# Kernel optimization log

Measured on AMD Instinct MI355X. Metric: run time of the kernel, lower is better.

## Reference

```python
import jax, jax.numpy as jnp
import numpy as np

EMBED_DIM = 768
HEAD_DIM = 64
BATCH = 8
SEQ = 4096


def setup_inputs() -> dict:
    key = jax.random.key(0)
    k_x, k_q, k_k, k_v = jax.random.split(key, 4)
    input_ids = jax.random.normal(k_x, (BATCH, SEQ, EMBED_DIM), dtype=jnp.float32)
    # nn.Linear(embed, head, bias=False): weight shape [head, embed]; y = x @ W.T
    scale = 1.0 / np.sqrt(EMBED_DIM)
    Wq = jax.random.normal(k_q, (HEAD_DIM, EMBED_DIM), dtype=jnp.float32) * scale
    Wk = jax.random.normal(k_k, (HEAD_DIM, EMBED_DIM), dtype=jnp.float32) * scale
    Wv = jax.random.normal(k_v, (HEAD_DIM, EMBED_DIM), dtype=jnp.float32) * scale
    return {"input_ids": input_ids, "Wq": Wq, "Wk": Wk, "Wv": Wv}


def reference(input_ids, Wq, Wk, Wv):
    # Projections. NOTE: the original module (faithfully reproduced) computes
    # v with q_net, so Wv is unused in the forward math.
    q = jnp.einsum('bse,he->bsh', input_ids, Wq)  # [B,S,H]
    k = jnp.einsum('bse,he->bsh', input_ids, Wk)  # [B,S,H]
    v = jnp.einsum('bse,he->bsh', input_ids, Wq)  # bug in source: uses q_net
    seq_len = q.shape[1]
    # Non-standard scaling: divide by sqrt(seq_len), not sqrt(head_dim)
    scores = jnp.einsum('bqh,bkh->bqk', q, k) / jnp.sqrt(jnp.float32(seq_len))
    # Non-standard softmax axis: over the query axis (dim=1)
    attn_weights = jax.nn.softmax(scores, axis=1)  # [B,Sq,Sk]
    return jnp.einsum('bqk,bkh->bqh', attn_weights, v)
```

## Files before the change

kernel.cpp:

```cpp
#include <hip/hip_runtime.h>
#include <hip/hip_bf16.h>
#include <cstdint>


#define BATCH 8
#define SEQ   4096
#define EMB   768
#define HD    64
#define NROW  (BATCH*SEQ)

#define QSCALE 0.1803368801111201f
#define KSCALE 0.125f
#define CSCALE 5.545177444479562f

typedef float  f32x4  __attribute__((ext_vector_type(4)));
typedef float  f32x16 __attribute__((ext_vector_type(16)));
typedef __bf16 bf16x8 __attribute__((ext_vector_type(8)));
typedef unsigned short u16x8_t __attribute__((ext_vector_type(8)));
typedef unsigned int   u32x4_t __attribute__((ext_vector_type(4)));

__device__ __forceinline__ f32x4 mfma16(bf16x8 a, bf16x8 b, f32x4 c) {
  return __builtin_amdgcn_mfma_f32_16x16x32_bf16(a, b, c, 0, 0, 0);
}
__device__ __forceinline__ f32x16 mfma32(bf16x8 a, bf16x8 b, f32x16 c) {
  return __builtin_amdgcn_mfma_f32_32x32x16_bf16(a, b, c, 0, 0, 0);
}
__device__ __forceinline__ unsigned short f2b(float f) {
  __bf16 h = (__bf16)f;
  return __builtin_bit_cast(unsigned short, h);
}
__device__ __forceinline__ float b2f(unsigned short u) {
  unsigned int x = ((unsigned int)u) << 16;
  return __builtin_bit_cast(float, x);
}
__device__ __forceinline__ bf16x8 ldsA(const unsigned short* p) {
  return __builtin_bit_cast(bf16x8, *(const u16x8_t*)p);
}
__device__ __forceinline__ float expf2(float x) {
  float r; asm("v_exp_f32 %0, %1" : "=v"(r) : "v"(x)); return r;
}
__device__ __forceinline__ unsigned cvtpk(float lo, float hi) {
  unsigned r; asm("v_cvt_pk_bf16_f32 %0, %1, %2" : "=v"(r) : "v"(lo), "v"(hi)); return r;
}
__device__ __forceinline__ void plane32swap(unsigned &a, unsigned &b) {
  asm volatile("v_permlane32_swap_b32 %0, %1" : "+v"(a), "+v"(b));
}
__device__ __forceinline__ void glld16(const void* g, void* l) {
  __builtin_amdgcn_global_load_lds(
      (const __attribute__((address_space(1))) void*)g,
      (__attribute__((address_space(3))) void*)l, 16, 0, 0);
}
__device__ __forceinline__ int sidx(int r, int h) {
  return r * 64 + (h ^ ((r & 7) << 3));
}

__global__ __launch_bounds__(256) void wcvt_kernel(
    const float* __restrict__ Wq, const float* __restrict__ Wk,
    unsigned short* __restrict__ Wb) {
  int ci = blockIdx.x * 256 + threadIdx.x;
  int r = ci / 96, c8 = ci % 96;
  const float* src = (r < 64 ? Wq + (size_t)r * EMB : Wk + (size_t)(r - 64) * EMB) + c8 * 8;
  float4 a = *(const float4*)src, d = *(const float4*)(src + 4);
  u16x8_t o;
  o[0]=f2b(a.x); o[1]=f2b(a.y); o[2]=f2b(a.z); o[3]=f2b(a.w);
  o[4]=f2b(d.x); o[5]=f2b(d.y); o[6]=f2b(d.z); o[7]=f2b(d.w);
  *(u16x8_t*)(Wb + (size_t)ci * 8) = o;
}

__global__ __launch_bounds__(256) void proj_kernel(
    const float* __restrict__ X, const unsigned short* __restrict__ Wb,
    unsigned short* __restrict__ Qb, unsigned short* __restrict__ Kb) {
  __shared__ unsigned short Ws[2][8192];
  const int t = threadIdx.x, lane = t & 63, w = t >> 6;
  const int c = lane & 15, g = lane >> 4;
  const int row0 = blockIdx.x * 64;
  f32x4 acc[8];
#pragma unroll
  for (int f = 0; f < 8; ++f) { acc[f][0]=0.f; acc[f][1]=0.f; acc[f][2]=0.f; acc[f][3]=0.f; }

  auto STAGE = [&](int ec, int bb) {
#pragma unroll
    for (int i = 0; i < 4; ++i) {
      int rr = w + 4 * i;
      int ci = rr * 64 + lane;
      int r = ci >> 3, cL = ci & 7;
      glld16(Wb + (size_t)r * EMB + ec * 64 + (cL ^ (r & 7)) * 8, (void*)&Ws[bb][rr * 512]);
    }
  };
  STAGE(0, 0);
  __syncthreads();
  for (int ec = 0; ec < 12; ++ec) {
    if (ec < 11) STAGE(ec + 1, (ec + 1) & 1);
    bf16x8 Af[2];
#pragma unroll
    for (int es = 0; es < 2; ++es) {
      const float* xp = X + (size_t)(row0 + 16 * w + c) * EMB + ec * 64 + es * 32 + 8 * g;
      float4 v0 = *(const float4*)xp, v1 = *(const float4*)(xp + 4);
      u16x8_t tmp;
      tmp[0]=f2b(v0.x); tmp[1]=f2b(v0.y); tmp[2]=f2b(v0.z); tmp[3]=f2b(v0.w);
      tmp[4]=f2b(v1.x); tmp[5]=f2b(v1.y); tmp[6]=f2b(v1.z); tmp[7]=f2b(v1.w);
      Af[es] = __builtin_bit_cast(bf16x8, tmp);
    }
    const unsigned short* Wt = Ws[ec & 1];
#pragma unroll
    for (int es = 0; es < 2; ++es)
#pragma unroll
      for (int f = 0; f < 8; ++f) {
        bf16x8 Bf = ldsA(&Wt[sidx(16 * f + c, es * 32 + 8 * g)]);
        acc[f] = mfma16(Af[es], Bf, acc[f]);
      }
    __syncthreads();
  }
#pragma unroll
  for (int f = 0; f < 8; ++f) {
    int n = 16 * f + c;
    float sc = (n < 64) ? QSCALE : KSCALE;
#pragma unroll
    for (int r = 0; r < 4; ++r) {
      int ROW = row0 + 16 * w + 4 * g + r;
      unsigned short bv = f2b(acc[f][r] * sc);
      if (n < 64) Qb[(size_t)ROW * 64 + n] = bv;
      else        Kb[(size_t)ROW * 64 + (n - 64)] = bv;
    }
  }
}

__global__ __launch_bounds__(256) void colsum_kernel(
    const unsigned short* __restrict__ Qb, const unsigned short* __restrict__ Kb,
    float* __restrict__ Zpart) {
  __shared__ unsigned short Qs[2][8192];
  const int t = threadIdx.x, lane = t & 63, w = t >> 6;
  const int c = lane & 31, hi = lane >> 5;
  const int fid = blockIdx.x;
  const int b = fid & 7, rem = fid >> 3;
  const int kt = rem & 15, qs = rem >> 4;
  const size_t kbase = (size_t)b * SEQ + kt * 256;
  const size_t qbase0 = (size_t)b * SEQ + qs * 1024;

  bf16x8 Kf[2][4];
#pragma unroll
  for (int j = 0; j < 2; ++j)
#pragma unroll
    for (int es = 0; es < 4; ++es)
      Kf[j][es] = __builtin_bit_cast(bf16x8,
          *(const u16x8_t*)(Kb + (kbase + 64 * w + 32 * j + c) * 64 + 16 * es + 8 * hi));

  auto STAGE = [&](int qi, int bb) {
#pragma unroll
    for (int i = 0; i < 4; ++i) {
      int rr = w + 4 * i;
      int ci = rr * 64 + lane;
      int r = ci >> 3, cL = ci & 7;
      glld16(Qb + (qbase0 + qi * 128 + r) * 64 + (cL ^ (r & 7)) * 8, (void*)&Qs[bb][rr * 512]);
    }
  };
  float csum[2] = {0.f, 0.f};
  STAGE(0, 0);
  __syncthreads();
  for (int qi = 0; qi < 8; ++qi) {
    if (qi < 7) STAGE(qi + 1, (qi + 1) & 1);
    const unsigned short* Qt = Qs[qi & 1];
#pragma unroll
    for (int sq = 0; sq < 4; ++sq) {
      bf16x8 A[4];
#pragma unroll
      for (int es = 0; es < 4; ++es)
        A[es] = ldsA(&Qt[sidx(32 * sq + c, 16 * es + 8 * hi)]);
#pragma unroll
      for (int j = 0; j < 2; ++j) {
        f32x16 sv;
#pragma unroll
        for (int i = 0; i < 16; ++i) sv[i] = 0.f;
#pragma unroll
        for (int es = 0; es < 4; ++es) sv = mfma32(A[es], Kf[j][es], sv);
#pragma unroll
        for (int i = 0; i < 16; ++i) csum[j] += expf2(sv[i]);
      }
    }
    __syncthreads();
  }
#pragma unroll
  for (int j = 0; j < 2; ++j) {
    float v = csum[j] + __shfl_xor(csum[j], 32);
    if (lane < 32)
      Zpart[(kbase + 64 * w + 32 * j + lane) * 4 + qs] = v;
  }
}

__global__ __launch_bounds__(256) void vtrans_kernel(
    const unsigned short* __restrict__ Qb, const float* __restrict__ Zpart,
    unsigned short* __restrict__ VT) {
  __shared__ unsigned short T[128 * 72];
  __shared__ float cvs[128];
  const int t = threadIdx.x;
  const int kt = blockIdx.x, b = blockIdx.y;
  const size_t kbase = (size_t)b * SEQ + kt * 128;
#pragma unroll
  for (int it = 0; it < 4; ++it) {
    int ci = t + 256 * it;
    int r = ci >> 3, ch = ci & 7;
    u16x8_t v = *(const u16x8_t*)(Qb + (kbase + r) * 64 + 8 * ch);
    *(u16x8_t*)(&T[r * 72 + 8 * (ch ^ ((r >> 3) & 7))]) = v;
  }
  if (t < 128) {
    const float* zp = Zpart + (kbase + t) * 4;
    cvs[t] = CSCALE / (zp[0] + zp[1] + zp[2] + zp[3]);
  }
  __syncthreads();
#pragma unroll
  for (int it = 0; it < 4; ++it) {
    int ci = t + 256 * it;
    int h = ci >> 4, c16 = ci & 15;
    u16x8_t o;
#pragma unroll
    for (int j = 0; j < 8; ++j) {
      int r = 8 * c16 + j;
      unsigned short raw = T[r * 72 + 8 * ((h >> 3) ^ (c16 & 7)) + (h & 7)];
      o[j] = f2b(cvs[r] * b2f(raw));
    }
    *(u16x8_t*)(VT + ((size_t)(b * 64 + h)) * SEQ + kt * 128 + 8 * c16) = o;
  }
}

__global__ __launch_bounds__(256) void attn_kernel(
    const unsigned short* __restrict__ Qb, const unsigned short* __restrict__ Kb,
    const unsigned short* __restrict__ VT, float* __restrict__ outp, int nkt) {
  __shared__ unsigned short KV[2][16384];
  const int t = threadIdx.x, lane = t & 63, w = t >> 6;
  const int c = lane & 31, hi = lane >> 5;
  const int fid = blockIdx.x;
  const int b = fid & 7, rem = fid >> 3;
  const int qt = rem & 15, ks = rem >> 4;
  const size_t brow = (size_t)b * SEQ;
  const int q0 = qt * 256;
  const int koff = ks * nkt;

  bf16x8 Qf[2][4];
#pragma unroll
  for (int j = 0; j < 2; ++j)
#pragma unroll
    for (int es = 0; es < 4; ++es)
      Qf[j][es] = __builtin_bit_cast(bf16x8,
          *(const u16x8_t*)(Qb + (brow + q0 + 64 * w + 32 * j + c) * 64 + 16 * es + 8 * hi));

  f32x16 acc[2][2];
#pragma unroll
  for (int j = 0; j < 2; ++j)
#pragma unroll
    for (int hb = 0; hb < 2; ++hb)
#pragma unroll
      for (int i = 0; i < 16; ++i) acc[j][hb][i] = 0.f;

  auto STAGE = [&](int tt, int bb) {
    const size_t kb0 = brow + (size_t)(koff + tt) * 128;
#pragma unroll
    for (int i = 0; i < 8; ++i) {
      int rr = w + 4 * i;
      int ci = rr * 64 + lane;
      if (rr < 16) {
        int r = ci >> 3, cL = ci & 7;
        glld16(Kb + (kb0 + r) * 64 + (cL ^ (r & 7)) * 8, (void*)&KV[bb][rr * 512]);
      } else {
        int jj = ci - 1024;
        int h = jj >> 4, cL = jj & 15;
        glld16(VT + ((size_t)(b * 64 + h)) * SEQ + (size_t)(koff + tt) * 128 +
                   (cL ^ (h & 7)) * 8,
               (void*)&KV[bb][rr * 512]);
      }
    }
  };

  auto COMPUTE = [&](int bb) {
    const unsigned short* Ks = &KV[bb][0];
    const unsigned short* Vs = &KV[bb][8192];
#pragma unroll
    for (int kb = 0; kb < 4; ++kb) {
      bf16x8 KA[4];
#pragma unroll
      for (int es = 0; es < 4; ++es)
        KA[es] = ldsA(&Ks[sidx(32 * kb + c, 16 * es + 8 * hi)]);
      bf16x8 fA[2][2];
#pragma unroll
      for (int j = 0; j < 2; ++j) {
        f32x16 sv;
#pragma unroll
        for (int i = 0; i < 16; ++i) sv[i] = 0.f;
#pragma unroll
        for (int es = 0; es < 4; ++es) sv = mfma32(KA[es], Qf[j][es], sv);
        float p[16];
#pragma unroll
        for (int i = 0; i < 16; ++i) p[i] = expf2(sv[i]);
        unsigned X0 = cvtpk(p[0], p[1]),  X1 = cvtpk(p[2], p[3]);
        unsigned Y0 = cvtpk(p[4], p[5]),  Y1 = cvtpk(p[6], p[7]);
        plane32swap(X0, Y0); plane32swap(X1, Y1);
        u32x4_t F0 = {X0, X1, Y0, Y1};
        unsigned Z0 = cvtpk(p[8], p[9]),   Z1 = cvtpk(p[10], p[11]);
        unsigned W0 = cvtpk(p[12], p[13]), W1 = cvtpk(p[14], p[15]);
        plane32swap(Z0, W0); plane32swap(Z1, W1);
        u32x4_t F1 = {Z0, Z1, W0, W1};
        fA[j][0] = __builtin_bit_cast(bf16x8, F0);
        fA[j][1] = __builtin_bit_cast(bf16x8, F1);
      }
#pragma unroll
      for (int hb = 0; hb < 2; ++hb) {
        int h = 32 * hb + c;
        int col0 = 32 * kb + 8 * hi;
        bf16x8 VB0 = ldsA(&Vs[h * 128 + (col0 ^ ((h & 7) << 3))]);
        bf16x8 VB1 = ldsA(&Vs[h * 128 + ((col0 + 16) ^ ((h & 7) << 3))]);
        acc[0][hb] = mfma32(fA[0][0], VB0, acc[0][hb]);
        acc[0][hb] = mfma32(fA[0][1], VB1, acc[0][hb]);
        acc[1][hb] = mfma32(fA[1][0], VB0, acc[1][hb]);
        acc[1][hb] = mfma32(fA[1][1], VB1, acc[1][hb]);
      }
    }
  };

  STAGE(0, 0);
  __syncthreads();
  for (int tt = 0; tt < nkt; ++tt) {
    if (tt + 1 < nkt) STAGE(tt + 1, (tt + 1) & 1);
    COMPUTE(tt & 1);
    __syncthreads();
  }
  float* op = outp + (size_t)ks * NROW * 64;
#pragma unroll
  for (int j = 0; j < 2; ++j)
#pragma unroll
    for (int hb = 0; hb < 2; ++hb)
#pragma unroll
      for (int r = 0; r < 16; ++r) {
        int qrow = (r & 3) + 8 * (r >> 2) + 4 * hi;
        op[(brow + q0 + 64 * w + 32 * j + qrow) * 64 + 32 * hb + c] = acc[j][hb][r];
      }
}

__global__ __launch_bounds__(256) void osum_kernel(
    const float4* __restrict__ A, const float4* __restrict__ B,
    const float4* __restrict__ C, const float4* __restrict__ D,
    float4* __restrict__ O) {
  int i = blockIdx.x * 256 + threadIdx.x;
  float4 x = A[i], y = B[i], z = C[i], u = D[i];
  float4 o;
  o.x = (x.x + y.x) + (z.x + u.x);
  o.y = (x.y + y.y) + (z.y + u.y);
  o.z = (x.z + y.z) + (z.z + u.z);
  o.w = (x.w + y.w) + (z.w + u.w);
  O[i] = o;
}

extern "C" void kernel_launch(void* const* d_in, const int* in_sizes, int n_in,
                              void* d_out, int out_size, void* d_ws, size_t ws_size,
                              hipStream_t stream) {
  const float* X  = (const float*)d_in[0];
  const float* Wq = (const float*)d_in[1];
  const float* Wk = (const float*)d_in[2];
  float* Out = (float*)d_out;

  unsigned char* wsb = (unsigned char*)d_ws;
  const size_t QB_OFF = 0;
  const size_t KB_OFF = 4194304;
  const size_t WB_OFF = 8388608;
  const size_t Z_OFF  = 8585216;
  const size_t VT_OFF = 9240576;
  const size_t OP_OFF = 13434880;
  const size_t TOTAL_SPLIT = OP_OFF + (size_t)4 * NROW * 64 * 4;

  unsigned short* Qb = (unsigned short*)(wsb + QB_OFF);
  unsigned short* Kb = (unsigned short*)(wsb + KB_OFF);
  unsigned short* Wb = (unsigned short*)(wsb + WB_OFF);
  float* Zpart       = (float*)(wsb + Z_OFF);
  unsigned short* VT = (unsigned short*)(wsb + VT_OFF);
  float* Opart       = (float*)(wsb + OP_OFF);

  const bool split = (ws_size >= TOTAL_SPLIT);

  hipLaunchKernelGGL(wcvt_kernel, dim3(48), dim3(256), 0, stream, Wq, Wk, Wb);
  hipLaunchKernelGGL(proj_kernel, dim3(NROW / 64), dim3(256), 0, stream, X, Wb, Qb, Kb);
  hipLaunchKernelGGL(colsum_kernel, dim3(512), dim3(256), 0, stream, Qb, Kb, Zpart);
  hipLaunchKernelGGL(vtrans_kernel, dim3(32, 8), dim3(256), 0, stream, Qb, Zpart, VT);
  if (split) {
    hipLaunchKernelGGL(attn_kernel, dim3(512), dim3(256), 0, stream,
                       Qb, Kb, VT, Opart, 8);
    const size_t PS = (size_t)NROW * 64;
    hipLaunchKernelGGL(osum_kernel, dim3(2048), dim3(256), 0, stream,
                       (const float4*)Opart, (const float4*)(Opart + PS),
                       (const float4*)(Opart + 2 * PS), (const float4*)(Opart + 3 * PS),
                       (float4*)Out);
  } else {
    hipLaunchKernelGGL(attn_kernel, dim3(128), dim3(256), 0, stream,
                       Qb, Kb, VT, Out, 32);
  }
}
```

Baseline: 105.5 us.

## Store split-K attention partials as fp16 and halve K/V tile size

The split-K attention kernel now writes its four partial outputs in fp16 instead of fp32, and the reduction kernel reads fp16 partials with 8-wide vector loads. This halves the partial-output traffic on both the write and the read side. The key/value LDS tile also shrinks from 128 to 64 keys per stage with twice as many iterations, which cuts shared memory per block and may allow more resident blocks, at the cost of more barriers. Rounding the partials to fp16 adds some precision loss.

```diff
diff --git a/kernel.cpp b/kernel.cpp
--- a/kernel.cpp
+++ b/kernel.cpp
@@ -33,7 +33,17 @@
   unsigned int x = ((unsigned int)u) << 16;
   return __builtin_bit_cast(float, x);
 }
+__device__ __forceinline__ unsigned short f2h(float f) {
+  _Float16 h = (_Float16)f;
+  return __builtin_bit_cast(unsigned short, h);
+}
+__device__ __forceinline__ float h2f(unsigned short u) {
+  return (float)__builtin_bit_cast(_Float16, u);
+}
 __device__ __forceinline__ bf16x8 ldsA(const unsigned short* p) {
+  return __builtin_bit_cast(bf16x8, *(const u16x8_t*)p);
+}
+__device__ __forceinline__ bf16x8 ldg8(const unsigned short* p) {
   return __builtin_bit_cast(bf16x8, *(const u16x8_t*)p);
 }
 __device__ __forceinline__ float expf2(float x) {
@@ -222,10 +232,11 @@
   }
 }
 
+template <bool F16P>
 __global__ __launch_bounds__(256) void attn_kernel(
     const unsigned short* __restrict__ Qb, const unsigned short* __restrict__ Kb,
-    const unsigned short* __restrict__ VT, float* __restrict__ outp, int nkt) {
-  __shared__ unsigned short KV[2][16384];
+    const unsigned short* __restrict__ VT, void* __restrict__ outp, int nkt) {
+  __shared__ unsigned short KV[2][8192];
   const int t = threadIdx.x, lane = t & 63, w = t >> 6;
   const int c = lane & 31, hi = lane >> 5;
   const int fid = blockIdx.x;
@@ -233,15 +244,15 @@
   const int qt = rem & 15, ks = rem >> 4;
   const size_t brow = (size_t)b * SEQ;
   const int q0 = qt * 256;
-  const int koff = ks * nkt;
+  const int ntiles = 2 * nkt;
+  const int t0 = ks * ntiles;
 
   bf16x8 Qf[2][4];
 #pragma unroll
   for (int j = 0; j < 2; ++j)
 #pragma unroll
     for (int es = 0; es < 4; ++es)
-      Qf[j][es] = __builtin_bit_cast(bf16x8,
-          *(const u16x8_t*)(Qb + (brow + q0 + 64 * w + 32 * j + c) * 64 + 16 * es + 8 * hi));
+      Qf[j][es] = ldg8(Qb + (brow + q0 + 64 * w + 32 * j + c) * 64 + 16 * es + 8 * hi);
 
   f32x16 acc[2][2];
 #pragma unroll
@@ -252,29 +263,29 @@
       for (int i = 0; i < 16; ++i) acc[j][hb][i] = 0.f;
 
   auto STAGE = [&](int tt, int bb) {
-    const size_t kb0 = brow + (size_t)(koff + tt) * 128;
-#pragma unroll
-    for (int i = 0; i < 8; ++i) {
+    const int k0 = (t0 + tt) * 64;
+    const size_t kb0 = brow + k0;
+#pragma unroll
+    for (int i = 0; i < 4; ++i) {
       int rr = w + 4 * i;
-      int ci = rr * 64 + lane;
-      if (rr < 16) {
+      if (rr < 8) {
+        int ci = rr * 64 + lane;
         int r = ci >> 3, cL = ci & 7;
         glld16(Kb + (kb0 + r) * 64 + (cL ^ (r & 7)) * 8, (void*)&KV[bb][rr * 512]);
       } else {
-        int jj = ci - 1024;
-        int h = jj >> 4, cL = jj & 15;
-        glld16(VT + ((size_t)(b * 64 + h)) * SEQ + (size_t)(koff + tt) * 128 +
-                   (cL ^ (h & 7)) * 8,
-               (void*)&KV[bb][rr * 512]);
+        int ci = (rr - 8) * 64 + lane;
+        int h = ci >> 3, cL = ci & 7;
+        glld16(VT + ((size_t)(b * 64 + h)) * SEQ + k0 + (cL ^ (h & 7)) * 8,
+               (void*)&KV[bb][4096 + (rr - 8) * 512]);
       }
     }
   };
 
   auto COMPUTE = [&](int bb) {
     const unsigned short* Ks = &KV[bb][0];
-    const unsigned short* Vs = &KV[bb][8192];
-#pragma unroll
-    for (int kb = 0; kb < 4; ++kb) {
+    const unsigned short* Vs = &KV[bb][4096];
+#pragma unroll
+    for (int kb = 0; kb < 2; ++kb) {
       bf16x8 KA[4];
 #pragma unroll
       for (int es = 0; es < 4; ++es)
@@ -305,8 +316,8 @@
       for (int hb = 0; hb < 2; ++hb) {
         int h = 32 * hb + c;
         int col0 = 32 * kb + 8 * hi;
-        bf16x8 VB0 = ldsA(&Vs[h * 128 + (col0 ^ ((h & 7) << 3))]);
-        bf16x8 VB1 = ldsA(&Vs[h * 128 + ((col0 + 16) ^ ((h & 7) << 3))]);
+        bf16x8 VB0 = ldsA(&Vs[h * 64 + (col0 ^ ((h & 7) << 3))]);
+        bf16x8 VB1 = ldsA(&Vs[h * 64 + ((col0 + 16) ^ ((h & 7) << 3))]);
         acc[0][hb] = mfma32(fA[0][0], VB0, acc[0][hb]);
         acc[0][hb] = mfma32(fA[0][1], VB1, acc[0][hb]);
         acc[1][hb] = mfma32(fA[1][0], VB0, acc[1][hb]);
@@ -317,12 +328,11 @@
 
   STAGE(0, 0);
   __syncthreads();
-  for (int tt = 0; tt < nkt; ++tt) {
-    if (tt + 1 < nkt) STAGE(tt + 1, (tt + 1) & 1);
+  for (int tt = 0; tt < ntiles; ++tt) {
+    if (tt + 1 < ntiles) STAGE(tt + 1, (tt + 1) & 1);
     COMPUTE(tt & 1);
     __syncthreads();
   }
-  float* op = outp + (size_t)ks * NROW * 64;
 #pragma unroll
   for (int j = 0; j < 2; ++j)
 #pragma unroll
@@ -330,22 +340,31 @@
 #pragma unroll
       for (int r = 0; r < 16; ++r) {
         int qrow = (r & 3) + 8 * (r >> 2) + 4 * hi;
-        op[(brow + q0 + 64 * w + 32 * j + qrow) * 64 + 32 * hb + c] = acc[j][hb][r];
+        size_t idx = (brow + q0 + 64 * w + 32 * j + qrow) * 64 + 32 * hb + c;
+        if (F16P) {
+          unsigned short* op = (unsigned short*)outp + (size_t)ks * NROW * 64;
+          op[idx] = f2h(acc[j][hb][r]);
+        } else {
+          ((float*)outp)[idx] = acc[j][hb][r];
+        }
       }
 }
 
 __global__ __launch_bounds__(256) void osum_kernel(
-    const float4* __restrict__ A, const float4* __restrict__ B,
-    const float4* __restrict__ C, const float4* __restrict__ D,
-    float4* __restrict__ O) {
-  int i = blockIdx.x * 256 + threadIdx.x;
-  float4 x = A[i], y = B[i], z = C[i], u = D[i];
-  float4 o;
-  o.x = (x.x + y.x) + (z.x + u.x);
-  o.y = (x.y + y.y) + (z.y + u.y);
-  o.z = (x.z + y.z) + (z.z + u.z);
-  o.w = (x.w + y.w) + (z.w + u.w);
-  O[i] = o;
+    const unsigned short* __restrict__ P, float* __restrict__ O) {
+  const size_t PS = (size_t)NROW * 64;
+  size_t i = ((size_t)blockIdx.x * 256 + threadIdx.x) * 8;
+  u16x8_t a = *(const u16x8_t*)(P + i);
+  u16x8_t b = *(const u16x8_t*)(P + PS + i);
+  u16x8_t c = *(const u16x8_t*)(P + 2 * PS + i);
+  u16x8_t d = *(const u16x8_t*)(P + 3 * PS + i);
+  float o[8];
+#pragma unroll
+  for (int j = 0; j < 8; ++j)
+    o[j] = (h2f(a[j]) + h2f(b[j])) + (h2f(c[j]) + h2f(d[j]));
+  float4 o0 = {o[0], o[1], o[2], o[3]}, o1 = {o[4], o[5], o[6], o[7]};
+  *(float4*)(O + i) = o0;
+  *(float4*)(O + i + 4) = o1;
 }
 
 extern "C" void kernel_launch(void* const* d_in, const int* in_sizes, int n_in,
@@ -363,14 +382,14 @@
   const size_t Z_OFF  = 8585216;
   const size_t VT_OFF = 9240576;
   const size_t OP_OFF = 13434880;
-  const size_t TOTAL_SPLIT = OP_OFF + (size_t)4 * NROW * 64 * 4;
+  const size_t TOTAL_SPLIT = OP_OFF + (size_t)4 * NROW * 64 * 2;
 
   unsigned short* Qb = (unsigned short*)(wsb + QB_OFF);
   unsigned short* Kb = (unsigned short*)(wsb + KB_OFF);
   unsigned short* Wb = (unsigned short*)(wsb + WB_OFF);
   float* Zpart       = (float*)(wsb + Z_OFF);
   unsigned short* VT = (unsigned short*)(wsb + VT_OFF);
-  float* Opart       = (float*)(wsb + OP_OFF);
+  unsigned short* OpH = (unsigned short*)(wsb + OP_OFF);
 
   const bool split = (ws_size >= TOTAL_SPLIT);
 
@@ -379,15 +398,11 @@
   hipLaunchKernelGGL(colsum_kernel, dim3(512), dim3(256), 0, stream, Qb, Kb, Zpart);
   hipLaunchKernelGGL(vtrans_kernel, dim3(32, 8), dim3(256), 0, stream, Qb, Zpart, VT);
   if (split) {
-    hipLaunchKernelGGL(attn_kernel, dim3(512), dim3(256), 0, stream,
-                       Qb, Kb, VT, Opart, 8);
-    const size_t PS = (size_t)NROW * 64;
-    hipLaunchKernelGGL(osum_kernel, dim3(2048), dim3(256), 0, stream,
-                       (const float4*)Opart, (const float4*)(Opart + PS),
-                       (const float4*)(Opart + 2 * PS), (const float4*)(Opart + 3 * PS),
-                       (float4*)Out);
+    hipLaunchKernelGGL(attn_kernel<true>, dim3(512), dim3(256), 0, stream,
+                       Qb, Kb, VT, (void*)OpH, 8);
+    hipLaunchKernelGGL(osum_kernel, dim3(1024), dim3(256), 0, stream, OpH, Out);
   } else {
-    hipLaunchKernelGGL(attn_kernel, dim3(128), dim3(256), 0, stream,
-                       Qb, Kb, VT, Out, 32);
-  }
-}
+    hipLaunchKernelGGL(attn_kernel<false>, dim3(128), dim3(256), 0, stream,
+                       Qb, Kb, VT, (void*)Out, 32);
+  }
+}
```

After: 104.3 us. About the same (-1.1%).
